# Kernel tuning notes

Measured on AMD Instinct MI355X. Metric: run time of the kernel, lower is better.

## Reference

```python
import jax, jax.numpy as jnp
import numpy as np

INPUT_SIZE = 1024
HIDDEN_SIZE = 1024
BATCH = 8192


def setup_inputs() -> dict:
    key = jax.random.key(0)
    ks = jax.random.split(key, 14)
    stdv = 1.0 / HIDDEN_SIZE ** 0.5
    u = lambda k, shape: jax.random.uniform(k, shape, jnp.float32, -stdv, stdv)
    H, I = HIDDEN_SIZE, INPUT_SIZE
    return {
        "x": jax.random.normal(ks[0], (BATCH, I), jnp.float32),
        "hidden": jax.random.normal(ks[1], (BATCH, H), jnp.float32),
        "weight_xr": u(ks[2], (H, I)),
        "weight_hr": u(ks[3], (H, H)),
        "bias_r": u(ks[4], (H,)),
        "weight_xz": u(ks[5], (H, I)),
        "weight_hz": u(ks[6], (H, H)),
        "bias_z": u(ks[7], (H,)),
        "weight_xh": u(ks[8], (H, I)),
        "weight_hh": u(ks[9], (H, H)),
        "bias_h": u(ks[10], (H,)),
        "weight_c": u(ks[11], (H, I + H)),
        "bias_c": u(ks[12], (H,)),
        "weight_hat_h": u(ks[13], (H, I + H)),
        "bias_hat_h": u(jax.random.fold_in(key, 99), (H,)),
    }


def reference(x, hidden, weight_xr, weight_hr, bias_r, weight_xz, weight_hz, bias_z,
              weight_xh, weight_hh, bias_h, weight_c, bias_c, weight_hat_h, bias_hat_h):
    # combined: [B, I+H]
    combined = jnp.concatenate([x, hidden], axis=1)
    c_t = combined @ weight_c.T + bias_c                      # [B, H]
    a_t = jax.nn.softmax(c_t, axis=1)
    hat_h_t = a_t * jax.nn.relu(combined @ weight_hat_h.T + bias_hat_h)
    r_t = jax.nn.sigmoid(x @ weight_xr.T + bias_r + hidden @ weight_hr.T)
    z_t = jax.nn.sigmoid(x @ weight_xz.T + bias_z + hidden @ weight_hz.T)
    h_tilde = jnp.tanh(x @ weight_xh.T + bias_h + (r_t * hidden) @ weight_hh.T)
    h_t = (1.0 - z_t) * h_tilde + z_t * hidden + hat_h_t
    return h_t
```

## Files before the change

### kernel.cpp

```cpp
#include <hip/hip_runtime.h>

typedef unsigned short ushort_t;
typedef __attribute__((ext_vector_type(8))) short short8;
typedef __attribute__((ext_vector_type(4))) float float4v;
typedef __attribute__((ext_vector_type(4))) ushort_t ushort4v;

#define B_ROWS 8192
#define HDIM   1024
#define GLD    5120

__device__ __forceinline__ float bf2f(ushort_t u) {
    return __uint_as_float(((unsigned)u) << 16);
}
__device__ __forceinline__ ushort_t f2bf(float f) {
    unsigned u = __float_as_uint(f);
    u += 0x7FFFu + ((u >> 16) & 1u);
    return (ushort_t)(u >> 16);
}

__global__ __launch_bounds__(256) void pack_all(
    const float* __restrict__ x, const float* __restrict__ h,
    const float* __restrict__ wc, const float* __restrict__ what,
    const float* __restrict__ wxr, const float* __restrict__ whr,
    const float* __restrict__ wxz, const float* __restrict__ whz,
    const float* __restrict__ wxh, const float* __restrict__ whh,
    ushort_t* __restrict__ A, ushort_t* __restrict__ W,
    ushort_t* __restrict__ Whh)
{
    const int bid = blockIdx.x;
    float4v v;
    ushort_t* dst;
    size_t i4;
    if (bid < 16384) {
        i4 = ((size_t)bid * 256 + threadIdx.x) * 4;
        int c = (int)(i4 & 2047);
        size_t b = i4 >> 11;
        const float* src = (c < 1024) ? (x + b * 1024 + c)
                                      : (h + b * 1024 + (c - 1024));
        v = *(const float4v*)src;
        dst = A + i4;
    } else if (bid < 26624) {
        i4 = ((size_t)(bid - 16384) * 256 + threadIdx.x) * 4;
        int j = (int)(i4 >> 11);
        int k = (int)(i4 & 2047);
        int r = j >> 10, jr = j & 1023;
        if (r == 0) {
            v = *(const float4v*)(wc + (size_t)j * 2048 + k);
        } else if (r == 1) {
            v = *(const float4v*)(what + (size_t)jr * 2048 + k);
        } else if (r == 4) {
            v = (k < 1024) ? *(const float4v*)(wxh + (size_t)jr * 1024 + k)
                           : (float4v){0.f, 0.f, 0.f, 0.f};
        } else {
            const float* p0 = (r == 2) ? wxr : wxz;
            const float* p1 = (r == 2) ? whr : whz;
            const float* p = (k < 1024) ? (p0 + (size_t)jr * 1024 + k)
                                        : (p1 + (size_t)jr * 1024 + (k - 1024));
            v = *(const float4v*)p;
        }
        dst = W + i4;
    } else {
        i4 = ((size_t)(bid - 26624) * 256 + threadIdx.x) * 4;
        v = *(const float4v*)(whh + i4);
        dst = Whh + i4;
    }
    ushort4v o;
#pragma unroll
    for (int t = 0; t < 4; ++t) o[t] = f2bf(v[t]);
    *(ushort4v*)dst = o;
}


#define GLOAD(gp, lp) __builtin_amdgcn_global_load_lds( \
    (const __attribute__((address_space(1))) void*)(gp), \
    (__attribute__((address_space(3))) void*)(lp), 16, 0, 0)

#define BARRIER __builtin_amdgcn_s_barrier()
#define WAITLGKM do { \
    asm volatile("s_waitcnt lgkmcnt(0)" ::: "memory"); \
    __builtin_amdgcn_sched_barrier(0); } while (0)
#define WAITVM6 do { \
    asm volatile("s_waitcnt vmcnt(6)" ::: "memory"); \
    __builtin_amdgcn_sched_barrier(0); } while (0)
#define WAITVM4 do { \
    asm volatile("s_waitcnt vmcnt(4)" ::: "memory"); \
    __builtin_amdgcn_sched_barrier(0); } while (0)
#define WAITVM0 do { \
    asm volatile("s_waitcnt vmcnt(0)" ::: "memory"); \
    __builtin_amdgcn_sched_barrier(0); } while (0)

#define STAGE_A(S, H, KT) do { \
    GLOAD(A + aS0 + (H) * 262144 + (KT) * 64, dstA + (S) * 32768 + (H) * 8192); \
    GLOAD(A + aS1 + (H) * 262144 + (KT) * 64, dstA + (S) * 32768 + (H) * 8192 + 512); } while (0)
#define STAGE_B(S, H, KT) do { \
    GLOAD(B + bS0 + (H) * 262144 + (KT) * 64, dstB + (S) * 32768 + (H) * 8192); \
    GLOAD(B + bS1 + (H) * 262144 + (KT) * 64, dstB + (S) * 32768 + (H) * 8192 + 512); } while (0)

#define LOAD_AF(S, H) do { \
    const ushort_t* _p = lds + (S) * 32768 + (H) * 8192 + aro; \
    _Pragma("unroll") \
    for (int mi = 0; mi < 4; ++mi) { \
        af0[mi] = *(const short8*)(_p + mi * 1024 + c0); \
        af1[mi] = *(const short8*)(_p + mi * 1024 + c1); } } while (0)

#define LOAD_BF(V0, V1, S, H) do { \
    const ushort_t* _p = lds + (S) * 32768 + 16384 + (H) * 8192 + bro; \
    _Pragma("unroll") \
    for (int ni = 0; ni < 2; ++ni) { \
        V0[ni] = *(const short8*)(_p + ni * 1024 + c0); \
        V1[ni] = *(const short8*)(_p + ni * 1024 + c1); } } while (0)

#define MFMA_Q(HA, HB, V0, V1) do { \
    __builtin_amdgcn_s_setprio(1); \
    _Pragma("unroll") \
    for (int mi = 0; mi < 4; ++mi) { \
        _Pragma("unroll") \
        for (int ni = 0; ni < 2; ++ni) { \
            acc[HA][HB][mi][ni] = __builtin_amdgcn_mfma_f32_16x16x32_bf16( \
                af0[mi], V0[ni], acc[HA][HB][mi][ni], 0, 0, 0); \
            acc[HA][HB][mi][ni] = __builtin_amdgcn_mfma_f32_16x16x32_bf16( \
                af1[mi], V1[ni], acc[HA][HB][mi][ni], 0, 0, 0); } } \
    __builtin_amdgcn_s_setprio(0); } while (0)

__global__ __launch_bounds__(512, 2) void gemm1(
    const ushort_t* __restrict__ A, const ushort_t* __restrict__ B,
    ushort_t* __restrict__ C)
{
    const int bid = blockIdx.x;
    int bx, by;
    if (bid < 512) { int hI = (bid & 7) * 64 + (bid >> 3); by = hI >> 4; bx = hI & 15; }
    else           { int b = bid - 512; int lI = (b & 7) * 16 + (b >> 3); by = lI >> 2; bx = 16 + (lI & 3); }
    const int bn0 = bx * 256;
    const int bm0 = by * 256;
    const int K = (bx >= 16) ? 1024 : 2048;
    const int NIT = K >> 7;

    __shared__ ushort_t lds[65536];

    const int t = threadIdx.x;
    const int w = t >> 6, lane = t & 63;
    const int wm2 = w >> 2, wn2 = w & 3;
    const int q = lane >> 4, r16 = lane & 15;

    const int c0 = ((q ^ (r16 & 7)) << 3);
    const int c1 = (((4 + q) ^ (r16 & 7)) << 3);
    const int aro = (wm2 * 64 + r16) * 64;
    const int bro = (wn2 * 32 + r16) * 64;

    const int srow0 = w * 16 + ((lane >> 3) & 7);
    const int kcO = ((lane & 7) ^ (lane >> 3)) << 3;
    const size_t aS0 = (size_t)(bm0 + srow0) * 2048 + kcO;
    const size_t aS1 = aS0 + 8 * 2048;
    const size_t bS0 = (size_t)(bn0 + srow0) * 2048 + kcO;
    const size_t bS1 = bS0 + 8 * 2048;
    ushort_t* dstA = lds + w * 1024;
    ushort_t* dstB = lds + 16384 + w * 1024;

    float4v acc[2][2][4][2];
#pragma unroll
    for (int i = 0; i < 2; ++i)
#pragma unroll
        for (int j = 0; j < 2; ++j)
#pragma unroll
            for (int m = 0; m < 4; ++m)
#pragma unroll
                for (int n = 0; n < 2; ++n)
                    acc[i][j][m][n] = {0.f, 0.f, 0.f, 0.f};

    short8 af0[4], af1[4];
    short8 b00[2], b01[2];
    short8 b10[2], b11[2];

    STAGE_A(0, 0, 0);
    STAGE_B(0, 0, 0);
    STAGE_A(0, 1, 0);
    STAGE_B(0, 1, 0);
    STAGE_A(1, 0, 1);
    STAGE_B(1, 1, 1);
    WAITVM4;
    BARRIER;

#pragma unroll 1
    for (int it = 0; it < NIT - 1; ++it) {
        const int kO  = 2 * it + 1;
        const int kE2 = 2 * it + 2;
        const int kO2 = 2 * it + 3;
        LOAD_AF(0, 0); LOAD_BF(b00, b01, 0, 0); STAGE_B(1, 0, kO);
        BARRIER; WAITLGKM; MFMA_Q(0, 0, b00, b01); WAITVM6; BARRIER;
        LOAD_BF(b10, b11, 0, 1); STAGE_A(1, 1, kO);
        BARRIER; WAITLGKM; MFMA_Q(0, 1, b10, b11); WAITVM6; BARRIER;
        LOAD_AF(0, 1); STAGE_A(0, 0, kE2);
        BARRIER; WAITLGKM; MFMA_Q(1, 1, b10, b11); WAITVM6; BARRIER;
        STAGE_B(0, 1, kE2);
        BARRIER; MFMA_Q(1, 0, b00, b01); WAITVM6; BARRIER;
        LOAD_AF(1, 0); LOAD_BF(b00, b01, 1, 0); STAGE_B(0, 0, kE2);
        BARRIER; WAITLGKM; MFMA_Q(0, 0, b00, b01); WAITVM6; BARRIER;
        LOAD_BF(b10, b11, 1, 1); STAGE_A(0, 1, kE2);
        BARRIER; WAITLGKM; MFMA_Q(0, 1, b10, b11); WAITVM6; BARRIER;
        LOAD_AF(1, 1); STAGE_A(1, 0, kO2);
        BARRIER; WAITLGKM; MFMA_Q(1, 1, b10, b11); WAITVM6; BARRIER;
        STAGE_B(1, 1, kO2);
        BARRIER; MFMA_Q(1, 0, b00, b01); WAITVM6; BARRIER;
    }

    {
        const int kO = 2 * (NIT - 1) + 1;
        LOAD_AF(0, 0); LOAD_BF(b00, b01, 0, 0); STAGE_B(1, 0, kO);
        BARRIER; WAITLGKM; MFMA_Q(0, 0, b00, b01); WAITVM6; BARRIER;
        LOAD_BF(b10, b11, 0, 1); STAGE_A(1, 1, kO);
        BARRIER; WAITLGKM; MFMA_Q(0, 1, b10, b11); WAITVM6; BARRIER;
        LOAD_AF(0, 1);
        WAITLGKM; MFMA_Q(1, 1, b10, b11);
        MFMA_Q(1, 0, b00, b01);
        WAITVM0;
        BARRIER;
        LOAD_AF(1, 0); LOAD_BF(b00, b01, 1, 0);
        WAITLGKM; MFMA_Q(0, 0, b00, b01);
        LOAD_BF(b10, b11, 1, 1);
        WAITLGKM; MFMA_Q(0, 1, b10, b11);
        LOAD_AF(1, 1);
        WAITLGKM; MFMA_Q(1, 1, b10, b11);
        MFMA_Q(1, 0, b00, b01);
    }

#pragma unroll
    for (int ha = 0; ha < 2; ++ha)
#pragma unroll
        for (int hb = 0; hb < 2; ++hb)
#pragma unroll
            for (int mi = 0; mi < 4; ++mi)
#pragma unroll
                for (int ni = 0; ni < 2; ++ni)
#pragma unroll
                    for (int reg = 0; reg < 4; ++reg) {
                        int row = bm0 + ha * 128 + wm2 * 64 + mi * 16 + q * 4 + reg;
                        int col = bn0 + hb * 128 + wn2 * 32 + ni * 16 + r16;
                        C[(size_t)row * GLD + col] = f2bf(acc[ha][hb][mi][ni][reg]);
                    }
}

__global__ __launch_bounds__(256) void row_pass(
    ushort_t* __restrict__ G, const float* __restrict__ bias_c,
    const float* __restrict__ bias_hat, const float* __restrict__ bias_r,
    const float* __restrict__ hidden, ushort_t* __restrict__ rh)
{
    const int wave = threadIdx.x >> 6, lane = threadIdx.x & 63;
    const size_t row = (size_t)blockIdx.x * 4 + wave;
    ushort_t* g = G + row * GLD;
    const int c0 = lane * 16;

    float cv[16];
    {
        short8 a = *(const short8*)(g + c0);
        short8 b = *(const short8*)(g + c0 + 8);
#pragma unroll
        for (int i = 0; i < 8; ++i) {
            cv[i]     = bf2f((ushort_t)a[i]) + bias_c[c0 + i];
            cv[8 + i] = bf2f((ushort_t)b[i]) + bias_c[c0 + 8 + i];
        }
    }
    float mx = cv[0];
#pragma unroll
    for (int i = 1; i < 16; ++i) mx = fmaxf(mx, cv[i]);
#pragma unroll
    for (int m = 1; m < 64; m <<= 1) mx = fmaxf(mx, __shfl_xor(mx, m));
    float sum = 0.f;
#pragma unroll
    for (int i = 0; i < 16; ++i) { cv[i] = __expf(cv[i] - mx); sum += cv[i]; }
#pragma unroll
    for (int m = 1; m < 64; m <<= 1) sum += __shfl_xor(sum, m);
    const float inv = 1.0f / sum;

    {
        short8 a = *(const short8*)(g + 1024 + c0);
        short8 b = *(const short8*)(g + 1024 + c0 + 8);
        short8 oa, ob;
#pragma unroll
        for (int i = 0; i < 8; ++i) {
            float ha = bf2f((ushort_t)a[i]) + bias_hat[c0 + i];
            float hb = bf2f((ushort_t)b[i]) + bias_hat[c0 + 8 + i];
            oa[i] = (short)f2bf(cv[i] * inv * fmaxf(ha, 0.f));
            ob[i] = (short)f2bf(cv[8 + i] * inv * fmaxf(hb, 0.f));
        }
        *(short8*)(g + c0) = oa;
        *(short8*)(g + c0 + 8) = ob;
    }

    {
        short8 a = *(const short8*)(g + 2048 + c0);
        short8 b = *(const short8*)(g + 2048 + c0 + 8);
        const float* hp = hidden + row * 1024 + c0;
        short8 oa, ob;
#pragma unroll
        for (int i = 0; i < 8; ++i) {
            float ra = 1.0f / (1.0f + __expf(-(bf2f((ushort_t)a[i]) + bias_r[c0 + i])));
            float rb = 1.0f / (1.0f + __expf(-(bf2f((ushort_t)b[i]) + bias_r[c0 + 8 + i])));
            oa[i] = (short)f2bf(ra * hp[i]);
            ob[i] = (short)f2bf(rb * hp[8 + i]);
        }
        ushort_t* rp = rh + row * 1024 + c0;
        *(short8*)rp = oa;
        *(short8*)(rp + 8) = ob;
    }
}

#define CSTRIDE 132
__global__ __launch_bounds__(256) void gemm2_final(
    const ushort_t* __restrict__ A, const ushort_t* __restrict__ B,
    const ushort_t* __restrict__ G, const float* __restrict__ bias_z,
    const float* __restrict__ bias_h, const float* __restrict__ hidden,
    float* __restrict__ out)
{
    const int bn0 = blockIdx.x * 128;
    const int bm0 = blockIdx.y * 64;

    __shared__ ushort_t smem[64 * CSTRIDE];
    ushort_t* As = smem;
    ushort_t* Bs = smem + 2048;

    const int t = threadIdx.x;
    const int wave = t >> 6, lane = t & 63;
    const int wr = wave >> 1, wcq = wave & 1;
    const int q = lane >> 4, r16 = lane & 15;
    const int lrow = lane >> 2;
    const int lcol = (lane & 3) * 8;

    float4v acc[2][4];
#pragma unroll
    for (int i = 0; i < 2; ++i)
#pragma unroll
        for (int j = 0; j < 4; ++j)
            acc[i][j] = {0.f, 0.f, 0.f, 0.f};

    for (int k0 = 0; k0 < 1024; k0 += 32) {
#pragma unroll
        for (int j = 0; j < 3; ++j) {
            int l = wave * 3 + j;
            if (l < 4) {
                const ushort_t* gp = A + (size_t)(bm0 + l * 16 + lrow) * 1024 + k0 + lcol;
                __builtin_amdgcn_global_load_lds(
                    (const __attribute__((address_space(1))) void*)gp,
                    (__attribute__((address_space(3))) void*)(As + l * 512),
                    16, 0, 0);
            } else {
                const ushort_t* gp = B + (size_t)(bn0 + (l - 4) * 16 + lrow) * 1024 + k0 + lcol;
                __builtin_amdgcn_global_load_lds(
                    (const __attribute__((address_space(1))) void*)gp,
                    (__attribute__((address_space(3))) void*)(Bs + (l - 4) * 512),
                    16, 0, 0);
            }
        }
        __syncthreads();

        short8 af[2], bf[4];
#pragma unroll
        for (int mi = 0; mi < 2; ++mi)
            af[mi] = *(const short8*)&As[(wr * 32 + mi * 16 + r16) * 32 + q * 8];
#pragma unroll
        for (int ni = 0; ni < 4; ++ni)
            bf[ni] = *(const short8*)&Bs[(wcq * 64 + ni * 16 + r16) * 32 + q * 8];
#pragma unroll
        for (int mi = 0; mi < 2; ++mi)
#pragma unroll
            for (int ni = 0; ni < 4; ++ni)
                acc[mi][ni] = __builtin_amdgcn_mfma_f32_16x16x32_bf16(
                    af[mi], bf[ni], acc[mi][ni], 0, 0, 0);
        __syncthreads();
    }

#pragma unroll
    for (int mi = 0; mi < 2; ++mi)
#pragma unroll
        for (int ni = 0; ni < 4; ++ni)
#pragma unroll
            for (int reg = 0; reg < 4; ++reg) {
                int rl = wr * 32 + mi * 16 + q * 4 + reg;
                int cl = wcq * 64 + ni * 16 + r16;
                smem[rl * CSTRIDE + cl] = f2bf(acc[mi][ni][reg]);
            }
    __syncthreads();

    const int colL = t & 127;
    const int gc = bn0 + colL;
    const float bz = bias_z[gc];
    const float bh = bias_h[gc];
    const int rbase = t >> 7;
#pragma unroll 4
    for (int pass = 0; pass < 32; ++pass) {
        const int rowL = pass * 2 + rbase;
        const size_t gr = (size_t)(bm0 + rowL);
        const ushort_t* grow = G + gr * GLD;
        float z = 1.0f / (1.0f + __expf(-(bf2f(grow[3072 + gc]) + bz)));
        float targ = bf2f(grow[4096 + gc]) + bh + bf2f(smem[rowL * CSTRIDE + colL]);
        float th = 1.0f - 2.0f / (__expf(2.0f * targ) + 1.0f);
        out[gr * 1024 + gc] =
            (1.0f - z) * th + z * hidden[gr * 1024 + gc] + bf2f(grow[gc]);
    }
}


extern "C" void kernel_launch(void* const* d_in, const int* in_sizes, int n_in,
                              void* d_out, int out_size, void* d_ws, size_t ws_size,
                              hipStream_t stream)
{
    const float* x        = (const float*)d_in[0];
    const float* hidden   = (const float*)d_in[1];
    const float* wxr      = (const float*)d_in[2];
    const float* whr      = (const float*)d_in[3];
    const float* bias_r   = (const float*)d_in[4];
    const float* wxz      = (const float*)d_in[5];
    const float* whz      = (const float*)d_in[6];
    const float* bias_z   = (const float*)d_in[7];
    const float* wxh      = (const float*)d_in[8];
    const float* whh      = (const float*)d_in[9];
    const float* bias_h   = (const float*)d_in[10];
    const float* wc       = (const float*)d_in[11];
    const float* bias_c   = (const float*)d_in[12];
    const float* what     = (const float*)d_in[13];
    const float* bias_hat = (const float*)d_in[14];
    float* out = (float*)d_out;

    char* ws = (char*)d_ws;
    ushort_t* G     = (ushort_t*)(ws);
    ushort_t* Abf   = (ushort_t*)(ws + 83886080);
    ushort_t* Wbf   = (ushort_t*)(ws + 117440512);
    ushort_t* Whhbf = (ushort_t*)(ws + 138412032);
    ushort_t* rhbf  = (ushort_t*)(ws + 140509184);

    pack_all<<<27648, 256, 0, stream>>>(x, hidden, wc, what, wxr, whr, wxz, whz,
                                        wxh, whh, Abf, Wbf, Whhbf);

    gemm1<<<640, 512, 0, stream>>>(Abf, Wbf, G);

    row_pass<<<B_ROWS / 4, 256, 0, stream>>>(G, bias_c, bias_hat, bias_r, hidden, rhbf);

    gemm2_final<<<dim3(8, 128), 256, 0, stream>>>(rhbf, Whhbf, G, bias_z, bias_h,
                                                  hidden, out);
}
```

Before: 358.3 us.

## Software-pipeline LDS fragment reads ahead of MFMA in gemm1 main loop

Restructures the gemm1 K-loop so the LDS fragment reads for the next quadrant are issued alongside the MFMAs of the current quadrant, using double-buffered A/B register fragments. This cuts the barrier-then-wait-then-compute serialization per quadrant. It also switches global offsets to 32-bit unsigned arithmetic to reduce address VALU work, and reorders the prologue loads. In exchange it uses more VGPRs for fragments, which could cause spills at 2 waves per SIMD, and the vmcnt and barrier accounting is more fragile.

```diff
diff --git a/kernel.cpp b/kernel.cpp
--- a/kernel.cpp
+++ b/kernel.cpp
@@ -75,51 +75,58 @@
     (const __attribute__((address_space(1))) void*)(gp), \
     (__attribute__((address_space(3))) void*)(lp), 16, 0, 0)
 
-#define BARRIER __builtin_amdgcn_s_barrier()
-#define WAITLGKM do { \
+#define BARRIER do { __builtin_amdgcn_s_barrier(); \
+    __builtin_amdgcn_sched_barrier(0); } while (0)
+#define WLG do { \
     asm volatile("s_waitcnt lgkmcnt(0)" ::: "memory"); \
     __builtin_amdgcn_sched_barrier(0); } while (0)
-#define WAITVM6 do { \
+#define WVM6 do { \
     asm volatile("s_waitcnt vmcnt(6)" ::: "memory"); \
     __builtin_amdgcn_sched_barrier(0); } while (0)
-#define WAITVM4 do { \
+#define WVM4 do { \
     asm volatile("s_waitcnt vmcnt(4)" ::: "memory"); \
     __builtin_amdgcn_sched_barrier(0); } while (0)
-#define WAITVM0 do { \
+#define WVM2 do { \
+    asm volatile("s_waitcnt vmcnt(2)" ::: "memory"); \
+    __builtin_amdgcn_sched_barrier(0); } while (0)
+#define WVM0 do { \
     asm volatile("s_waitcnt vmcnt(0)" ::: "memory"); \
     __builtin_amdgcn_sched_barrier(0); } while (0)
 
 #define STAGE_A(S, H, KT) do { \
-    GLOAD(A + aS0 + (H) * 262144 + (KT) * 64, dstA + (S) * 32768 + (H) * 8192); \
-    GLOAD(A + aS1 + (H) * 262144 + (KT) * 64, dstA + (S) * 32768 + (H) * 8192 + 512); } while (0)
+    GLOAD(A + (aO0 + (H) * 262144u + (unsigned)(KT) * 64u), dstA + (S) * 32768 + (H) * 8192); \
+    GLOAD(A + (aO1 + (H) * 262144u + (unsigned)(KT) * 64u), dstA + (S) * 32768 + (H) * 8192 + 512); } while (0)
 #define STAGE_B(S, H, KT) do { \
-    GLOAD(B + bS0 + (H) * 262144 + (KT) * 64, dstB + (S) * 32768 + (H) * 8192); \
-    GLOAD(B + bS1 + (H) * 262144 + (KT) * 64, dstB + (S) * 32768 + (H) * 8192 + 512); } while (0)
-
-#define LOAD_AF(S, H) do { \
-    const ushort_t* _p = lds + (S) * 32768 + (H) * 8192 + aro; \
+    GLOAD(B + (bO0 + (H) * 262144u + (unsigned)(KT) * 64u), dstB + (S) * 32768 + (H) * 8192); \
+    GLOAD(B + (bO1 + (H) * 262144u + (unsigned)(KT) * 64u), dstB + (S) * 32768 + (H) * 8192 + 512); } while (0)
+
+#define RD_A(BK, S, H) do { \
     _Pragma("unroll") \
     for (int mi = 0; mi < 4; ++mi) { \
-        af0[mi] = *(const short8*)(_p + mi * 1024 + c0); \
-        af1[mi] = *(const short8*)(_p + mi * 1024 + c1); } } while (0)
-
-#define LOAD_BF(V0, V1, S, H) do { \
-    const ushort_t* _p = lds + (S) * 32768 + 16384 + (H) * 8192 + bro; \
+        BK[mi]     = *(const short8*)(lds + (S) * 32768 + (H) * 8192 + mi * 1024 + Ard0); \
+        BK[4 + mi] = *(const short8*)(lds + (S) * 32768 + (H) * 8192 + mi * 1024 + Ard1); } } while (0)
+
+#define RD_A_KH(BK, S, H, KH) do { \
+    _Pragma("unroll") \
+    for (int mi = 0; mi < 4; ++mi) \
+        BK[(KH) * 4 + mi] = *(const short8*)(lds + (S) * 32768 + (H) * 8192 + mi * 1024 + ((KH) ? Ard1 : Ard0)); } while (0)
+
+#define RD_B(BK, S, H) do { \
     _Pragma("unroll") \
     for (int ni = 0; ni < 2; ++ni) { \
-        V0[ni] = *(const short8*)(_p + ni * 1024 + c0); \
-        V1[ni] = *(const short8*)(_p + ni * 1024 + c1); } } while (0)
-
-#define MFMA_Q(HA, HB, V0, V1) do { \
+        BK[ni]     = *(const short8*)(lds + (S) * 32768 + 16384 + (H) * 8192 + ni * 1024 + Brd0); \
+        BK[2 + ni] = *(const short8*)(lds + (S) * 32768 + 16384 + (H) * 8192 + ni * 1024 + Brd1); } } while (0)
+
+#define MM(HA, HB, AB, BB) do { \
     __builtin_amdgcn_s_setprio(1); \
     _Pragma("unroll") \
     for (int mi = 0; mi < 4; ++mi) { \
         _Pragma("unroll") \
         for (int ni = 0; ni < 2; ++ni) { \
             acc[HA][HB][mi][ni] = __builtin_amdgcn_mfma_f32_16x16x32_bf16( \
-                af0[mi], V0[ni], acc[HA][HB][mi][ni], 0, 0, 0); \
+                AB[mi], BB[ni], acc[HA][HB][mi][ni], 0, 0, 0); \
             acc[HA][HB][mi][ni] = __builtin_amdgcn_mfma_f32_16x16x32_bf16( \
-                af1[mi], V1[ni], acc[HA][HB][mi][ni], 0, 0, 0); } } \
+                AB[4 + mi], BB[2 + ni], acc[HA][HB][mi][ni], 0, 0, 0); } } \
     __builtin_amdgcn_s_setprio(0); } while (0)
 
 __global__ __launch_bounds__(512, 2) void gemm1(
@@ -139,20 +146,21 @@
 
     const int t = threadIdx.x;
     const int w = t >> 6, lane = t & 63;
-    const int wm2 = w >> 2, wn2 = w & 3;
     const int q = lane >> 4, r16 = lane & 15;
 
     const int c0 = ((q ^ (r16 & 7)) << 3);
     const int c1 = (((4 + q) ^ (r16 & 7)) << 3);
-    const int aro = (wm2 * 64 + r16) * 64;
-    const int bro = (wn2 * 32 + r16) * 64;
-
-    const int srow0 = w * 16 + ((lane >> 3) & 7);
-    const int kcO = ((lane & 7) ^ (lane >> 3)) << 3;
-    const size_t aS0 = (size_t)(bm0 + srow0) * 2048 + kcO;
-    const size_t aS1 = aS0 + 8 * 2048;
-    const size_t bS0 = (size_t)(bn0 + srow0) * 2048 + kcO;
-    const size_t bS1 = bS0 + 8 * 2048;
+    const int Ard0 = ((w >> 2) * 64 + r16) * 64 + c0;
+    const int Ard1 = ((w >> 2) * 64 + r16) * 64 + c1;
+    const int Brd0 = ((w & 3) * 32 + r16) * 64 + c0;
+    const int Brd1 = ((w & 3) * 32 + r16) * 64 + c1;
+
+    const unsigned srow0 = (unsigned)(w * 16 + ((lane >> 3) & 7));
+    const unsigned kcO = (unsigned)(((lane & 7) ^ (lane >> 3)) << 3);
+    const unsigned aO0 = ((unsigned)bm0 + srow0) * 2048u + kcO;
+    const unsigned aO1 = aO0 + 8u * 2048u;
+    const unsigned bO0 = ((unsigned)bn0 + srow0) * 2048u + kcO;
+    const unsigned bO1 = bO0 + 8u * 2048u;
     ushort_t* dstA = lds + w * 1024;
     ushort_t* dstB = lds + 16384 + w * 1024;
 
@@ -167,76 +175,107 @@
                 for (int n = 0; n < 2; ++n)
                     acc[i][j][m][n] = {0.f, 0.f, 0.f, 0.f};
 
-    short8 af0[4], af1[4];
-    short8 b00[2], b01[2];
-    short8 b10[2], b11[2];
+    short8 fX[8], fY[8];
+    short8 gA[4], gB[4];
 
     STAGE_A(0, 0, 0);
+    STAGE_B(0, 1, 0);
     STAGE_B(0, 0, 0);
     STAGE_A(0, 1, 0);
-    STAGE_B(0, 1, 0);
     STAGE_A(1, 0, 1);
     STAGE_B(1, 1, 1);
-    WAITVM4;
+    WVM4;
     BARRIER;
+    RD_A(fX, 0, 0);
+    RD_B(gA, 0, 0);
 
 #pragma unroll 1
     for (int it = 0; it < NIT - 1; ++it) {
         const int kO  = 2 * it + 1;
         const int kE2 = 2 * it + 2;
         const int kO2 = 2 * it + 3;
-        LOAD_AF(0, 0); LOAD_BF(b00, b01, 0, 0); STAGE_B(1, 0, kO);
-        BARRIER; WAITLGKM; MFMA_Q(0, 0, b00, b01); WAITVM6; BARRIER;
-        LOAD_BF(b10, b11, 0, 1); STAGE_A(1, 1, kO);
-        BARRIER; WAITLGKM; MFMA_Q(0, 1, b10, b11); WAITVM6; BARRIER;
-        LOAD_AF(0, 1); STAGE_A(0, 0, kE2);
-        BARRIER; WAITLGKM; MFMA_Q(1, 1, b10, b11); WAITVM6; BARRIER;
+        WLG; BARRIER;
+        STAGE_B(1, 0, kO);
+        RD_B(gB, 0, 1);
+        MM(0, 0, fX, gA);
+        WVM6; WLG; BARRIER;
+        STAGE_A(1, 1, kO);
+        RD_A(fY, 0, 1);
+        MM(0, 1, fX, gB);
+        WVM6; WLG; BARRIER;
+        STAGE_A(0, 0, kE2);
+        RD_A_KH(fX, 1, 0, 0);
+        MM(1, 1, fY, gB);
+        WVM4; WLG; BARRIER;
         STAGE_B(0, 1, kE2);
-        BARRIER; MFMA_Q(1, 0, b00, b01); WAITVM6; BARRIER;
-        LOAD_AF(1, 0); LOAD_BF(b00, b01, 1, 0); STAGE_B(0, 0, kE2);
-        BARRIER; WAITLGKM; MFMA_Q(0, 0, b00, b01); WAITVM6; BARRIER;
-        LOAD_BF(b10, b11, 1, 1); STAGE_A(0, 1, kE2);
-        BARRIER; WAITLGKM; MFMA_Q(0, 1, b10, b11); WAITVM6; BARRIER;
-        LOAD_AF(1, 1); STAGE_A(1, 0, kO2);
-        BARRIER; WAITLGKM; MFMA_Q(1, 1, b10, b11); WAITVM6; BARRIER;
+        RD_A_KH(fX, 1, 0, 1);
+        RD_B(gB, 1, 0);
+        MM(1, 0, fY, gA);
+        WLG; BARRIER;
+        STAGE_B(0, 0, kE2);
+        RD_B(gA, 1, 1);
+        MM(0, 0, fX, gB);
+        WVM6; WLG; BARRIER;
+        STAGE_A(0, 1, kE2);
+        RD_A(fY, 1, 1);
+        MM(0, 1, fX, gA);
+        WVM6; WLG; BARRIER;
+        STAGE_A(1, 0, kO2);
+        RD_A_KH(fX, 0, 0, 0);
+        MM(1, 1, fY, gA);
+        WVM4; WLG; BARRIER;
         STAGE_B(1, 1, kO2);
-        BARRIER; MFMA_Q(1, 0, b00, b01); WAITVM6; BARRIER;
+        RD_A_KH(fX, 0, 0, 1);
+        RD_B(gA, 0, 0);
+        MM(1, 0, fY, gB);
     }
 
     {
         const int kO = 2 * (NIT - 1) + 1;
-        LOAD_AF(0, 0); LOAD_BF(b00, b01, 0, 0); STAGE_B(1, 0, kO);
-        BARRIER; WAITLGKM; MFMA_Q(0, 0, b00, b01); WAITVM6; BARRIER;
-        LOAD_BF(b10, b11, 0, 1); STAGE_A(1, 1, kO);
-        BARRIER; WAITLGKM; MFMA_Q(0, 1, b10, b11); WAITVM6; BARRIER;
-        LOAD_AF(0, 1);
-        WAITLGKM; MFMA_Q(1, 1, b10, b11);
-        MFMA_Q(1, 0, b00, b01);
-        WAITVM0;
-        BARRIER;
-        LOAD_AF(1, 0); LOAD_BF(b00, b01, 1, 0);
-        WAITLGKM; MFMA_Q(0, 0, b00, b01);
-        LOAD_BF(b10, b11, 1, 1);
-        WAITLGKM; MFMA_Q(0, 1, b10, b11);
-        LOAD_AF(1, 1);
-        WAITLGKM; MFMA_Q(1, 1, b10, b11);
-        MFMA_Q(1, 0, b00, b01);
-    }
-
-#pragma unroll
-    for (int ha = 0; ha < 2; ++ha)
-#pragma unroll
-        for (int hb = 0; hb < 2; ++hb)
-#pragma unroll
-            for (int mi = 0; mi < 4; ++mi)
-#pragma unroll
-                for (int ni = 0; ni < 2; ++ni)
-#pragma unroll
-                    for (int reg = 0; reg < 4; ++reg) {
-                        int row = bm0 + ha * 128 + wm2 * 64 + mi * 16 + q * 4 + reg;
-                        int col = bn0 + hb * 128 + wn2 * 32 + ni * 16 + r16;
-                        C[(size_t)row * GLD + col] = f2bf(acc[ha][hb][mi][ni][reg]);
-                    }
+        WLG; BARRIER;
+        STAGE_B(1, 0, kO);
+        RD_B(gB, 0, 1);
+        MM(0, 0, fX, gA);
+        WVM6; WLG; BARRIER;
+        STAGE_A(1, 1, kO);
+        RD_A(fY, 0, 1);
+        MM(0, 1, fX, gB);
+        WVM6; WLG; BARRIER;
+        RD_A_KH(fX, 1, 0, 0);
+        MM(1, 1, fY, gB);
+        WVM2; WLG; BARRIER;
+        RD_A_KH(fX, 1, 0, 1);
+        RD_B(gB, 1, 0);
+        MM(1, 0, fY, gA);
+        WLG; BARRIER;
+        RD_B(gA, 1, 1);
+        MM(0, 0, fX, gB);
+        WVM0; WLG; BARRIER;
+        RD_A(fY, 1, 1);
+        MM(0, 1, fX, gA);
+        WLG; BARRIER;
+        MM(1, 1, fY, gA);
+        WLG; BARRIER;
+        MM(1, 0, fY, gB);
+    }
+
+    {
+        const int wm2 = w >> 2, wn2 = w & 3;
+#pragma unroll
+        for (int ha = 0; ha < 2; ++ha)
+#pragma unroll
+            for (int hb = 0; hb < 2; ++hb)
+#pragma unroll
+                for (int mi = 0; mi < 4; ++mi)
+#pragma unroll
+                    for (int ni = 0; ni < 2; ++ni)
+#pragma unroll
+                        for (int reg = 0; reg < 4; ++reg) {
+                            int row = bm0 + ha * 128 + wm2 * 64 + mi * 16 + q * 4 + reg;
+                            int col = bn0 + hb * 128 + wn2 * 32 + ni * 16 + r16;
+                            C[(size_t)row * GLD + col] = f2bf(acc[ha][hb][mi][ni][reg]);
+                        }
+    }
 }
 
 __global__ __launch_bounds__(256) void row_pass(
```

After: 406.3 us. 13.4% more time.
